# Kernel tuning notes

Measured on AMD Instinct MI355X. Metric: run time of the kernel, lower is better.

Reference implementation:

```python
import jax, jax.numpy as jnp
import numpy as np

B = 524288   # number of samples scored at inference
K = 8        # GMM mixture components
D = 16       # latent feature dim (AE code + reconstruction-error features)


def setup_inputs() -> dict:
    key = jax.random.key(0)
    k1, k2, k3, k4 = jax.random.split(key, 4)
    z = jax.random.normal(k1, (B, D), dtype=jnp.float32)
    mu = jax.random.normal(k2, (K, D), dtype=jnp.float32)
    # sigma must be SPD (it is an estimated covariance + 0.001*I in the original);
    # build it as A A^T / D + 0.1*I so cholesky succeeds and densities are sane.
    A = jax.random.normal(k3, (K, D, D), dtype=jnp.float32) / np.sqrt(D)
    sigma = jnp.einsum('kij,klj->kil', A, A) + 0.1 * jnp.eye(D, dtype=jnp.float32)
    logits = jax.random.normal(k4, (K,), dtype=jnp.float32)
    mixture_probabilities = jax.nn.softmax(logits)
    return {"mu": mu, "sigma": sigma, "z": z,
            "mixture_probabilities": mixture_probabilities}


def reference(mu, sigma, z, mixture_probabilities):
    # Faithful to compute_sample_energy: per-sample MVN density for each of K
    # components via Cholesky, weighted by mixture probs, summed, -log.
    # Vectorized: one batched triangular solve instead of tf.map_fn per sample.
    d = z.shape[-1]
    L = jnp.linalg.cholesky(sigma)                      # [K,D,D]
    diff = z[:, None, :] - mu[None, :, :]               # [B,K,D]
    diff_t = jnp.transpose(diff, (1, 2, 0))             # [K,D,B]
    y = jax.scipy.linalg.solve_triangular(L, diff_t, lower=True)  # [K,D,B]
    maha = jnp.sum(y * y, axis=1)                       # [K,B] Mahalanobis dist
    log_det = jnp.sum(jnp.log(jnp.diagonal(L, axis1=-2, axis2=-1)), axis=-1)  # [K]
    log_norm = -0.5 * d * jnp.log(jnp.asarray(2.0 * np.pi, dtype=z.dtype))
    log_prob = log_norm - log_det[:, None] - 0.5 * maha  # [K,B]
    densities = jnp.exp(log_prob).T                      # [B,K] == map_fn(prob)
    energy = -jnp.log(jnp.sum(densities * mixture_probabilities, axis=1))  # [B]
    return energy
```

## Files before the change

kernel.cpp:

```cpp
#include <hip/hip_runtime.h>
#include <math.h>

#define KCOMP 8
#define DDIM  16
#define UNR   4


__global__ __launch_bounds__(128) void prep_kernel(
    const float* __restrict__ mu, const float* __restrict__ sigma,
    const float* __restrict__ pi, float* __restrict__ ws)
{
    __shared__ float sLinv[KCOMP * DDIM * DDIM];
    const int tid = threadIdx.x;
    const int g = tid >> 4;
    const int r = tid & 15;

    float a[DDIM];
    const float4* srow = (const float4*)(sigma + g * DDIM * DDIM + r * DDIM);
    float4 v0 = srow[0], v1 = srow[1], v2 = srow[2], v3 = srow[3];
    a[0]=v0.x;  a[1]=v0.y;  a[2]=v0.z;  a[3]=v0.w;
    a[4]=v1.x;  a[5]=v1.y;  a[6]=v1.z;  a[7]=v1.w;
    a[8]=v2.x;  a[9]=v2.y;  a[10]=v2.z; a[11]=v2.w;
    a[12]=v3.x; a[13]=v3.y; a[14]=v3.z; a[15]=v3.w;

    float l[DDIM];
    #pragma unroll
    for (int j = 0; j < DDIM; ++j) {
        float s = a[j];
        #pragma unroll
        for (int m = 0; m < j; ++m)
            s -= l[m] * __shfl(l[m], j, DDIM);
        float dj = sqrtf(__shfl(s, j, DDIM));
        float val;
        if (r == j)      val = dj;
        else if (r > j)  val = s / dj;
        else             val = 0.0f;
        l[j] = val;
    }

    float x[DDIM];
    #pragma unroll
    for (int i = 0; i < DDIM; ++i) {
        float t = (r == i) ? 1.0f : 0.0f;
        #pragma unroll
        for (int m = 0; m < i; ++m)
            t -= __shfl(l[m], i, DDIM) * x[m];
        x[i] = t / __shfl(l[i], i, DDIM);
    }

    #pragma unroll
    for (int i = 0; i < DDIM; ++i) {
        sLinv[g * 256 + i * DDIM + r] = x[i];
        ws[g * 256 + i * DDIM + r]    = x[i];
    }
    __syncthreads();

    float b = 0.0f;
    #pragma unroll
    for (int c = 0; c < DDIM; ++c)
        b += sLinv[g * 256 + r * DDIM + c] * mu[g * DDIM + c];
    ws[KCOMP * 256 + g * DDIM + r] = b;

    float ld = logf(l[r]);
    #pragma unroll
    for (int off = 8; off >= 1; off >>= 1)
        ld += __shfl_xor(ld, off, DDIM);
    if (r == 0) {
        const float LOG2PI = 1.8378770664093454f;
        float ck = logf(pi[g]) - ld - 0.5f * DDIM * LOG2PI;
        ws[KCOMP * 256 + KCOMP * DDIM + g] = ck;
    }
}

__global__ __launch_bounds__(256) void energy_kernel(
    const float* __restrict__ z, const float* __restrict__ ws,
    float* __restrict__ out, int n)
{
    __shared__ __align__(16) float sL[KCOMP * DDIM * DDIM];
    __shared__ __align__(16) float sB[KCOMP * DDIM];
    __shared__ float sC[KCOMP];

    const int NPREP = KCOMP * 256 + KCOMP * DDIM + KCOMP;
    for (int t = threadIdx.x; t < NPREP; t += 256) {
        float v = ws[t];
        if (t < KCOMP * 256)                  sL[t] = v;
        else if (t < KCOMP * 256 + KCOMP*16)  sB[t - KCOMP * 256] = v;
        else                                  sC[t - KCOMP * 256 - KCOMP * 16] = v;
    }
    __syncthreads();

    const int stride = gridDim.x * 256;
    const int tid0 = blockIdx.x * 256 + threadIdx.x;

    float d[UNR][DDIM];
    int   s[UNR];
    bool  ok[UNR];
    #pragma unroll
    for (int u = 0; u < UNR; ++u) {
        s[u] = tid0 + u * stride;
        ok[u] = (s[u] < n);
        if (ok[u]) {
            const float4* zp = (const float4*)(z + (size_t)s[u] * DDIM);
            float4 w0 = zp[0], w1 = zp[1], w2 = zp[2], w3 = zp[3];
            d[u][0]=w0.x;  d[u][1]=w0.y;  d[u][2]=w0.z;  d[u][3]=w0.w;
            d[u][4]=w1.x;  d[u][5]=w1.y;  d[u][6]=w1.z;  d[u][7]=w1.w;
            d[u][8]=w2.x;  d[u][9]=w2.y;  d[u][10]=w2.z; d[u][11]=w2.w;
            d[u][12]=w3.x; d[u][13]=w3.y; d[u][14]=w3.z; d[u][15]=w3.w;
        } else {
            #pragma unroll
            for (int c = 0; c < DDIM; ++c) d[u][c] = 0.0f;
        }
    }

    float mx[UNR], dens[UNR];
    #pragma unroll
    for (int u = 0; u < UNR; ++u) { mx[u] = -1e30f; dens[u] = 0.0f; }

    #pragma unroll 1
    for (int k = 0; k < KCOMP; ++k) {
        const float* Lk = &sL[k * 256];
        float maha[UNR];
        #pragma unroll
        for (int u = 0; u < UNR; ++u) maha[u] = 0.0f;

        #pragma unroll
        for (int i = 0; i < DDIM; ++i) {
            float bi = sB[k * DDIM + i];
            float y[UNR];
            #pragma unroll
            for (int u = 0; u < UNR; ++u) y[u] = -bi;
            #pragma unroll
            for (int c = 0; c <= i; ++c) {
                float lv = Lk[i * DDIM + c];
                #pragma unroll
                for (int u = 0; u < UNR; ++u) y[u] = fmaf(lv, d[u][c], y[u]);
            }
            #pragma unroll
            for (int u = 0; u < UNR; ++u) maha[u] = fmaf(y[u], y[u], maha[u]);
        }
        float ck = sC[k];
        #pragma unroll
        for (int u = 0; u < UNR; ++u) {
            float lp = fmaf(-0.5f, maha[u], ck);
            float nm = fmaxf(mx[u], lp);
            dens[u] = dens[u] * __expf(mx[u] - nm) + __expf(lp - nm);
            mx[u] = nm;
        }
    }

    #pragma unroll
    for (int u = 0; u < UNR; ++u)
        if (ok[u]) out[s[u]] = -(mx[u] + __logf(dens[u]));
}

extern "C" void kernel_launch(void* const* d_in, const int* in_sizes, int n_in,
                              void* d_out, int out_size, void* d_ws, size_t ws_size,
                              hipStream_t stream) {
    const float* mu    = (const float*)d_in[0];
    const float* sigma = (const float*)d_in[1];
    const float* z     = (const float*)d_in[2];
    const float* pi    = (const float*)d_in[3];
    float* ws  = (float*)d_ws;
    float* out = (float*)d_out;

    const int n = in_sizes[2] / DDIM;

    prep_kernel<<<1, 128, 0, stream>>>(mu, sigma, pi, ws);

    const int blocks = (n + 256 * UNR - 1) / (256 * UNR);
    energy_kernel<<<blocks, 256, 0, stream>>>(z, ws, out, n);
}
```

Before: 110.6 us.

## Compute Mahalanobis transform with bf16 MFMA instead of scalar FMA loops

New measurement: 106.4 us. -3.8%, faster.

```diff
diff --git a/kernel.cpp b/kernel.cpp
--- a/kernel.cpp
+++ b/kernel.cpp
@@ -3,7 +3,15 @@
 
 #define KCOMP 8
 #define DDIM  16
-#define UNR   4
+
+typedef __attribute__((ext_vector_type(8))) short bf16x8;
+typedef __attribute__((ext_vector_type(4))) float f32x4;
+
+static __device__ __forceinline__ short f2bf(float f) {
+    unsigned u = __float_as_uint(f);
+    unsigned r = (u + 0x7FFFu + ((u >> 16) & 1u)) >> 16;
+    return (short)r;
+}
 
 
 __global__ __launch_bounds__(128) void prep_kernel(
@@ -76,81 +84,78 @@
     const float* __restrict__ z, const float* __restrict__ ws,
     float* __restrict__ out, int n)
 {
-    __shared__ __align__(16) float sL[KCOMP * DDIM * DDIM];
-    __shared__ __align__(16) float sB[KCOMP * DDIM];
-    __shared__ float sC[KCOMP];
+    const int lane = threadIdx.x & 63;
+    const int m    = lane & 15;
+    const int quad = lane >> 4;
+    const int wave = (blockIdx.x * blockDim.x + threadIdx.x) >> 6;
 
-    const int NPREP = KCOMP * 256 + KCOMP * DDIM + KCOMP;
-    for (int t = threadIdx.x; t < NPREP; t += 256) {
-        float v = ws[t];
-        if (t < KCOMP * 256)                  sL[t] = v;
-        else if (t < KCOMP * 256 + KCOMP*16)  sB[t - KCOMP * 256] = v;
-        else                                  sC[t - KCOMP * 256 - KCOMP * 16] = v;
+    bf16x8 afrag[KCOMP];
+    #pragma unroll
+    for (int k = 0; k < KCOMP; ++k) {
+        bf16x8 a = {0,0,0,0,0,0,0,0};
+        if (quad < 2) {
+            const float* Lrow = ws + k * 256 + m * DDIM + quad * 8;
+            #pragma unroll
+            for (int j = 0; j < 8; ++j) a[j] = f2bf(Lrow[j]);
+        } else if (quad == 2) {
+            a[0] = f2bf(-ws[KCOMP * 256 + k * DDIM + m]);
+        }
+        afrag[k] = a;
     }
-    __syncthreads();
+    float ck[KCOMP];
+    #pragma unroll
+    for (int k = 0; k < KCOMP; ++k)
+        ck[k] = ws[KCOMP * 256 + KCOMP * DDIM + k];
 
-    const int stride = gridDim.x * 256;
-    const int tid0 = blockIdx.x * 256 + threadIdx.x;
-
-    float d[UNR][DDIM];
-    int   s[UNR];
-    bool  ok[UNR];
-    #pragma unroll
-    for (int u = 0; u < UNR; ++u) {
-        s[u] = tid0 + u * stride;
-        ok[u] = (s[u] < n);
-        if (ok[u]) {
-            const float4* zp = (const float4*)(z + (size_t)s[u] * DDIM);
-            float4 w0 = zp[0], w1 = zp[1], w2 = zp[2], w3 = zp[3];
-            d[u][0]=w0.x;  d[u][1]=w0.y;  d[u][2]=w0.z;  d[u][3]=w0.w;
-            d[u][4]=w1.x;  d[u][5]=w1.y;  d[u][6]=w1.z;  d[u][7]=w1.w;
-            d[u][8]=w2.x;  d[u][9]=w2.y;  d[u][10]=w2.z; d[u][11]=w2.w;
-            d[u][12]=w3.x; d[u][13]=w3.y; d[u][14]=w3.z; d[u][15]=w3.w;
-        } else {
-            #pragma unroll
-            for (int c = 0; c < DDIM; ++c) d[u][c] = 0.0f;
-        }
-    }
-
-    float mx[UNR], dens[UNR];
-    #pragma unroll
-    for (int u = 0; u < UNR; ++u) { mx[u] = -1e30f; dens[u] = 0.0f; }
+    const f32x4 zero4 = {0.f, 0.f, 0.f, 0.f};
+    const int SPW = 256;
+    const int base = wave * SPW;
 
     #pragma unroll 1
-    for (int k = 0; k < KCOMP; ++k) {
-        const float* Lk = &sL[k * 256];
-        float maha[UNR];
+    for (int it = 0; it < SPW / 64; ++it) {
+        const int tb = base + it * 64;
+        float en[4];
         #pragma unroll
-        for (int u = 0; u < UNR; ++u) maha[u] = 0.0f;
+        for (int t = 0; t < 4; ++t) {
+            bf16x8 bfrag = {0,0,0,0,0,0,0,0};
+            const int s = tb + t * 16 + m;
+            if (quad < 2) {
+                if (s < n) {
+                    const float* zp = z + (size_t)s * DDIM + quad * 8;
+                    #pragma unroll
+                    for (int j = 0; j < 8; ++j) bfrag[j] = f2bf(zp[j]);
+                }
+            } else if (quad == 2) {
+                bfrag[0] = (short)0x3F80;
+            }
 
-        #pragma unroll
-        for (int i = 0; i < DDIM; ++i) {
-            float bi = sB[k * DDIM + i];
-            float y[UNR];
+            f32x4 dres[KCOMP];
             #pragma unroll
-            for (int u = 0; u < UNR; ++u) y[u] = -bi;
+            for (int k = 0; k < KCOMP; ++k)
+                dres[k] = __builtin_amdgcn_mfma_f32_16x16x32_bf16(
+                              afrag[k], bfrag, zero4, 0, 0, 0);
+
+            float mx = -1e30f, dens = 0.0f;
             #pragma unroll
-            for (int c = 0; c <= i; ++c) {
-                float lv = Lk[i * DDIM + c];
-                #pragma unroll
-                for (int u = 0; u < UNR; ++u) y[u] = fmaf(lv, d[u][c], y[u]);
+            for (int k = 0; k < KCOMP; ++k) {
+                f32x4 d4 = dres[k];
+                float p = d4[0]*d4[0] + d4[1]*d4[1] + d4[2]*d4[2] + d4[3]*d4[3];
+                p += __shfl_xor(p, 16, 64);
+                p += __shfl_xor(p, 32, 64);
+                float lp = fmaf(-0.5f, p, ck[k]);
+                float nm = fmaxf(mx, lp);
+                dens = dens * __expf(mx - nm) + __expf(lp - nm);
+                mx = nm;
             }
-            #pragma unroll
-            for (int u = 0; u < UNR; ++u) maha[u] = fmaf(y[u], y[u], maha[u]);
+            en[t] = -(mx + __logf(dens));
         }
-        float ck = sC[k];
-        #pragma unroll
-        for (int u = 0; u < UNR; ++u) {
-            float lp = fmaf(-0.5f, maha[u], ck);
-            float nm = fmaxf(mx[u], lp);
-            dens[u] = dens[u] * __expf(mx[u] - nm) + __expf(lp - nm);
-            mx[u] = nm;
-        }
+        float e = en[0];
+        e = (quad == 1) ? en[1] : e;
+        e = (quad == 2) ? en[2] : e;
+        e = (quad == 3) ? en[3] : e;
+        const int so = tb + quad * 16 + m;
+        if (so < n) out[so] = e;
     }
-
-    #pragma unroll
-    for (int u = 0; u < UNR; ++u)
-        if (ok[u]) out[s[u]] = -(mx[u] + __logf(dens[u]));
 }
 
 extern "C" void kernel_launch(void* const* d_in, const int* in_sizes, int n_in,
@@ -167,6 +172,6 @@
 
     prep_kernel<<<1, 128, 0, stream>>>(mu, sigma, pi, ws);
 
-    const int blocks = (n + 256 * UNR - 1) / (256 * UNR);
+    const int blocks = (n + 1023) / 1024;
     energy_kernel<<<blocks, 256, 0, stream>>>(z, ws, out, n);
 }
```
